# Optimization experiments

Hardware: AMD Instinct MI355X
Metric: run time of the kernel (lower is better)

The kernel has to match this reference:

```python
import jax, jax.numpy as jnp
import numpy as np

GMAX = 1.0   # args.gmax
GMIN = 0.01  # args.gmin
EPS = 0.1    # args.e_train


def setup_inputs() -> dict:
    key = jax.random.key(0)
    k1, k2, k3, k4 = jax.random.split(key, 4)
    N, B, NIN, NOUT, E = 8, 32, 128, 128, 1024
    # analog signals live in [0, 1]
    a_previous = jax.random.uniform(k1, (N, B, NIN, E), dtype=jnp.float32)
    # conductance params (clamped to [-gmax, gmax] in forward)
    theta = jax.random.uniform(k2, (NIN + 2, NOUT), dtype=jnp.float32) * 2.0 - 1.0
    # per-replica multiplicative noise seed in [0, 1); forward maps to 1 +- eps
    noise = jax.random.uniform(k3, (N, NIN + 2, NOUT), dtype=jnp.float32)
    # printed-tanh activation params eta = [offset, scale, shift, slope]
    eta = jnp.array([0.0, 1.0, 0.0, 1.0], dtype=jnp.float32) + 0.1 * jax.random.normal(k4, (4,), dtype=jnp.float32)
    return {"a_previous": a_previous, "theta": theta, "noise": noise, "eta": eta}


def reference(a_previous, theta, noise, eta):
    sg = jax.lax.stop_gradient
    # theta property: clamp + gmin pruning with straight-through estimator
    t = jnp.clip(theta, -GMAX, GMAX)
    t = jnp.where(jnp.abs(t) < GMIN, 0.0, t)
    theta_eff = sg(t) + theta - sg(theta)
    # theta_noisy: replicate over N with multiplicative uniform noise in [1-eps, 1+eps]
    theta_noisy = theta_eff[None, :, :] * ((noise * 2.0 - 1.0) * EPS + 1.0)  # [N, M, O], M = n_in+2
    # W: abs-normalized conductances per output column group
    abs_tn = jnp.abs(theta_noisy)
    W = abs_tn / (jnp.sum(abs_tn, axis=1, keepdims=True) + 1e-10)
    # sign masks (constants w.r.t. grad: values fully overwritten in torch)
    pos = sg((theta_noisy >= 0.0).astype(theta_noisy.dtype))
    neg = 1.0 - pos
    # a: [N, B, n_in, E] -> [N, B, E, n_in]; append ones and zeros columns
    a_r = jnp.transpose(a_previous, (0, 1, 3, 2))
    ones = jnp.ones(a_r.shape[:3] + (1,), a_r.dtype)
    zeros = jnp.zeros_like(ones)
    a_ext = jnp.concatenate([a_r, ones, zeros], axis=3)  # [N, B, E, M]
    # INV: unipolar complement; zero the last (zeros) column after inversion
    a_neg = (1.0 - a_ext).at[..., -1].set(0.0)
    # split-sign MAC: z [N, B, E, n_out]
    z = (jnp.einsum('nbem,nmo->nbeo', a_ext, W * pos)
         + jnp.einsum('nbem,nmo->nbeo', a_neg, W * neg))
    # printed tanh activation
    act = eta[0] + eta[1] * jnp.tanh((z - eta[2]) * eta[3])
    # back to [N, B, n_out, E]
    return jnp.transpose(act, (0, 1, 3, 2))
```

## Files before the change

kernel.cpp:

```cpp
#include <hip/hip_runtime.h>
#include <hip/hip_bf16.h>
#include <stdint.h>

#define N_REP 8
#define BATCH 32
#define NIN   128
#define NOUT  128
#define EDIM  1024
#define MDIM  130
#define ETILE 128
#define SE    130

typedef __attribute__((ext_vector_type(8))) short short8;
typedef __attribute__((ext_vector_type(4))) float f32x4;

__device__ __forceinline__ unsigned short f2bf(float f) {
    union { float f; uint32_t u; } v;
    v.f = f;
    uint32_t u = v.u;
    uint32_t r = u + 0x7fffu + ((u >> 16) & 1u);
    return (unsigned short)(r >> 16);
}

__device__ __forceinline__ uint32_t pk2bf(float lo, float hi) {
    __hip_bfloat162 h = __float22bfloat162_rn(make_float2(lo, hi));
    uint32_t d;
    __builtin_memcpy(&d, &h, 4);
    return d;
}

__global__ __launch_bounds__(64)
void prep_kernel(const float* __restrict__ theta,
                 const float* __restrict__ noise,
                 unsigned short* __restrict__ Sg,
                 float* __restrict__ biasg) {
    const int n = blockIdx.x >> 7;
    const int o = blockIdx.x & 127;
    const int lane = threadIdx.x;

    const float* nb = noise + (size_t)n * MDIM * NOUT + o;
    auto tn_at = [&](int m) -> float {
        float t = theta[m * NOUT + o];
        t = fminf(fmaxf(t, -1.f), 1.f);
        if (fabsf(t) < 0.01f) t = 0.f;
        return t * fmaf(nb[m * NOUT], 0.2f, 0.9f);
    };

    const float t0 = tn_at(lane);
    const float t1 = tn_at(lane + 64);
    const float t2 = (lane < 2) ? tn_at(128 + lane) : 0.f;

    float s = fabsf(t0) + fabsf(t1) + fabsf(t2);
#pragma unroll
    for (int d = 1; d < 64; d <<= 1) s += __shfl_xor(s, d, 64);
    const float inv = 1.f / (s + 1e-10f);

    const float w0 = fabsf(t0) * inv, w1 = fabsf(t1) * inv;
    unsigned short* srow = Sg + ((size_t)n * NOUT + o) * NIN;
    srow[lane]      = f2bf(t0 >= 0.f ? w0 : -w0);
    srow[lane + 64] = f2bf(t1 >= 0.f ? w1 : -w1);

    float b = (t0 < 0.f ? w0 : 0.f) + (t1 < 0.f ? w1 : 0.f);
    if (lane == 0 && t2 >= 0.f) b += fabsf(t2) * inv;
#pragma unroll
    for (int d = 1; d < 64; d <<= 1) b += __shfl_xor(b, d, 64);
    if (lane == 0) biasg[n * NOUT + o] = b;
}

__global__ __launch_bounds__(256, 4)
void gemm_kernel(const float* __restrict__ a,
                 const unsigned short* __restrict__ Sg,
                 const float* __restrict__ biasg,
                 const float* __restrict__ eta,
                 float* __restrict__ out) {
    __shared__ uint32_t Alds[64 * SE];
    const int bid = blockIdx.x;
    const int et  = bid & 7;
    const int nb  = bid >> 3;
    const int n   = nb >> 5;
    const int tid = threadIdx.x;

    {
        const float* abase = a + (size_t)nb * (NIN * EDIM) + et * ETILE;
        const int e4  = (tid & 31) << 2;
        const int mp0 = tid >> 5;
#pragma unroll
        for (int it = 0; it < 8; ++it) {
            const int mp = mp0 + (it << 3);
            const float4 va = *(const float4*)(abase + (size_t)(2 * mp) * EDIM + e4);
            const float4 vb = *(const float4*)(abase + (size_t)(2 * mp + 1) * EDIM + e4);
            uint2 d0, d1;
            d0.x = pk2bf(va.x, vb.x);
            d0.y = pk2bf(va.y, vb.y);
            d1.x = pk2bf(va.z, vb.z);
            d1.y = pk2bf(va.w, vb.w);
            *(uint2*)&Alds[mp * SE + e4]     = d0;
            *(uint2*)&Alds[mp * SE + e4 + 2] = d1;
        }
    }
    __syncthreads();

    const int lane = tid & 63;
    const int w = tid >> 6;
    const int r = lane & 15;
    const int q = lane >> 4;
    const int o_base = (w & 1) << 6;
    const int e_base = (w >> 1) << 6;

    f32x4 acc[4][4];
#pragma unroll
    for (int fo = 0; fo < 4; ++fo)
#pragma unroll
        for (int fe = 0; fe < 4; ++fe)
            acc[fo][fe] = (f32x4){0.f, 0.f, 0.f, 0.f};

#pragma unroll
    for (int ks = 0; ks < 4; ++ks) {
        short8 sf[4];
#pragma unroll
        for (int fo = 0; fo < 4; ++fo) {
            const int o = o_base + (fo << 4) + r;
            sf[fo] = *(const short8*)(Sg + ((size_t)(n * NOUT + o) << 7) + (ks << 5) + (q << 3));
        }
        short8 af[4];
        const int mpb = (ks << 4) + (q << 2);
#pragma unroll
        for (int fe = 0; fe < 4; ++fe) {
            const int e = e_base + (fe << 4) + r;
            uint32_t d[4];
#pragma unroll
            for (int jj = 0; jj < 4; ++jj)
                d[jj] = Alds[(mpb + jj) * SE + e];
            __builtin_memcpy(&af[fe], d, 16);
        }
#pragma unroll
        for (int fo = 0; fo < 4; ++fo)
#pragma unroll
            for (int fe = 0; fe < 4; ++fe)
                acc[fo][fe] = __builtin_amdgcn_mfma_f32_16x16x32_bf16(
                    sf[fo], af[fe], acc[fo][fe], 0, 0, 0);
    }

    const float e0 = eta[0], e1 = eta[1], e2 = eta[2], e3 = eta[3];
    float* obase = out + (size_t)nb * (NOUT * EDIM) + et * ETILE;
#pragma unroll
    for (int fo = 0; fo < 4; ++fo) {
        const int orow0 = o_base + (fo << 4) + (q << 2);
        const float4 bias4 = *(const float4*)(biasg + n * NOUT + orow0);
        const float bv[4] = {bias4.x, bias4.y, bias4.z, bias4.w};
#pragma unroll
        for (int i = 0; i < 4; ++i) {
            float* orow = obase + (size_t)(orow0 + i) * EDIM;
#pragma unroll
            for (int fe = 0; fe < 4; ++fe) {
                const float z = acc[fo][fe][i] + bv[i];
                const float y = (z - e2) * e3;
                const float ex = __expf(2.f * y);
                const float th = 1.f - 2.f * __builtin_amdgcn_rcpf(ex + 1.f);
                orow[e_base + (fe << 4) + r] = fmaf(e1, th, e0);
            }
        }
    }
}

extern "C" void kernel_launch(void* const* d_in, const int* in_sizes, int n_in,
                              void* d_out, int out_size, void* d_ws, size_t ws_size,
                              hipStream_t stream) {
    const float* a     = (const float*)d_in[0];
    const float* theta = (const float*)d_in[1];
    const float* noise = (const float*)d_in[2];
    const float* eta   = (const float*)d_in[3];
    float* out = (float*)d_out;

    unsigned short* Sg = (unsigned short*)d_ws;
    float* biasg = (float*)((char*)d_ws + (size_t)N_REP * NOUT * NIN * sizeof(unsigned short));

    prep_kernel<<<N_REP * NOUT, 64, 0, stream>>>(theta, noise, Sg, biasg);
    gemm_kernel<<<N_REP * BATCH * (EDIM / ETILE), 256, 0, stream>>>(a, Sg, biasg, eta, out);
}
```

Before: 254.3 us.

## Load A tile directly to LDS, halve E tile, vectorize output stores

Loads the fp32 activation tile with global_load_lds straight into shared memory, skipping the register round-trip, and converts to bf16 only when building MFMA fragments. ETILE is halved to 64, doubling the block count, and the MFMA operands are swapped so each lane holds four consecutive E outputs and can store them as one float4. The next k-step's weight fragments are prefetched, and bias and eta loads are hoisted ahead of the barrier. The trade-off is fp32 data in LDS (more LDS traffic, conversion inside the inner loop) and more weight reloads per output across the smaller tiles.

```diff
diff --git a/kernel.cpp b/kernel.cpp
--- a/kernel.cpp
+++ b/kernel.cpp
@@ -8,8 +8,9 @@
 #define NOUT  128
 #define EDIM  1024
 #define MDIM  130
-#define ETILE 128
-#define SE    130
+#define ETILE 64
+#define NGRP  32
+#define GSTR  260
 
 typedef __attribute__((ext_vector_type(8))) short short8;
 typedef __attribute__((ext_vector_type(4))) float f32x4;
@@ -27,6 +28,12 @@
     uint32_t d;
     __builtin_memcpy(&d, &h, 4);
     return d;
+}
+
+__device__ __forceinline__ void gload_lds16(float* lds, const float* g) {
+    __builtin_amdgcn_global_load_lds(
+        (const __attribute__((address_space(1))) void*)g,
+        (__attribute__((address_space(3))) void*)lds, 16, 0, 0);
 }
 
 __global__ __launch_bounds__(64)
@@ -73,92 +80,103 @@
                  const float* __restrict__ biasg,
                  const float* __restrict__ eta,
                  float* __restrict__ out) {
-    __shared__ uint32_t Alds[64 * SE];
-    const int bid = blockIdx.x;
-    const int et  = bid & 7;
-    const int nb  = bid >> 3;
-    const int n   = nb >> 5;
-    const int tid = threadIdx.x;
+    __shared__ float Alds[NGRP * GSTR];
+    const int bid  = blockIdx.x;
+    const int et   = bid & 15;
+    const int nb   = bid >> 4;
+    const int n    = nb >> 5;
+    const int tid  = threadIdx.x;
+    const int lane = tid & 63;
+    const int w    = tid >> 6;
+    const int r    = lane & 15;
+    const int q    = lane >> 4;
 
     {
-        const float* abase = a + (size_t)nb * (NIN * EDIM) + et * ETILE;
-        const int e4  = (tid & 31) << 2;
-        const int mp0 = tid >> 5;
+        const float* gp = a + (size_t)nb * (NIN * EDIM)
+                            + (size_t)(w * 32 + q) * EDIM + et * ETILE + (r << 2);
+        float* lp = &Alds[(w * 8) * GSTR];
 #pragma unroll
-        for (int it = 0; it < 8; ++it) {
-            const int mp = mp0 + (it << 3);
-            const float4 va = *(const float4*)(abase + (size_t)(2 * mp) * EDIM + e4);
-            const float4 vb = *(const float4*)(abase + (size_t)(2 * mp + 1) * EDIM + e4);
-            uint2 d0, d1;
-            d0.x = pk2bf(va.x, vb.x);
-            d0.y = pk2bf(va.y, vb.y);
-            d1.x = pk2bf(va.z, vb.z);
-            d1.y = pk2bf(va.w, vb.w);
-            *(uint2*)&Alds[mp * SE + e4]     = d0;
-            *(uint2*)&Alds[mp * SE + e4 + 2] = d1;
-        }
+        for (int t = 0; t < 8; ++t)
+            gload_lds16(lp + t * GSTR, gp + (size_t)(t * 4) * EDIM);
     }
-    __syncthreads();
 
-    const int lane = tid & 63;
-    const int w = tid >> 6;
-    const int r = lane & 15;
-    const int q = lane >> 4;
     const int o_base = (w & 1) << 6;
-    const int e_base = (w >> 1) << 6;
+    const int e_base = (w >> 1) << 5;
 
-    f32x4 acc[4][4];
+    const float e0 = eta[0], e1 = eta[1], e2 = eta[2], e3 = eta[3];
+    float bl[4];
+#pragma unroll
+    for (int fo = 0; fo < 4; ++fo)
+        bl[fo] = biasg[n * NOUT + o_base + (fo << 4) + r];
+
+    const unsigned short* sbase = Sg + ((size_t)(n * NOUT) << 7) + (q << 3);
+    short8 sf[4];
+#pragma unroll
+    for (int fo = 0; fo < 4; ++fo)
+        sf[fo] = *(const short8*)(sbase + ((size_t)(o_base + (fo << 4) + r) << 7));
+
+    f32x4 acc[4][2];
 #pragma unroll
     for (int fo = 0; fo < 4; ++fo)
 #pragma unroll
-        for (int fe = 0; fe < 4; ++fe)
+        for (int fe = 0; fe < 2; ++fe)
             acc[fo][fe] = (f32x4){0.f, 0.f, 0.f, 0.f};
+
+    __syncthreads();
 
 #pragma unroll
     for (int ks = 0; ks < 4; ++ks) {
-        short8 sf[4];
+        short8 sfn[4];
+        if (ks < 3) {
 #pragma unroll
-        for (int fo = 0; fo < 4; ++fo) {
-            const int o = o_base + (fo << 4) + r;
-            sf[fo] = *(const short8*)(Sg + ((size_t)(n * NOUT + o) << 7) + (ks << 5) + (q << 3));
+            for (int fo = 0; fo < 4; ++fo)
+                sfn[fo] = *(const short8*)(sbase + ((size_t)(o_base + (fo << 4) + r) << 7)
+                                                 + ((ks + 1) << 5));
         }
-        short8 af[4];
-        const int mpb = (ks << 4) + (q << 2);
+        short8 af[2];
 #pragma unroll
-        for (int fe = 0; fe < 4; ++fe) {
-            const int e = e_base + (fe << 4) + r;
+        for (int fe = 0; fe < 2; ++fe) {
+            const float* base = &Alds[(ks * 8 + q * 2) * GSTR + e_base + (fe << 4) + r];
             uint32_t d[4];
 #pragma unroll
-            for (int jj = 0; jj < 4; ++jj)
-                d[jj] = Alds[(mpb + jj) * SE + e];
+            for (int t = 0; t < 4; ++t) {
+                const int j0 = 2 * t, j1 = 2 * t + 1;
+                const float f0 = base[(j0 >> 2) * GSTR + (j0 & 3) * 64];
+                const float f1 = base[(j1 >> 2) * GSTR + (j1 & 3) * 64];
+                d[t] = pk2bf(f0, f1);
+            }
             __builtin_memcpy(&af[fe], d, 16);
         }
 #pragma unroll
         for (int fo = 0; fo < 4; ++fo)
 #pragma unroll
-            for (int fe = 0; fe < 4; ++fe)
+            for (int fe = 0; fe < 2; ++fe)
                 acc[fo][fe] = __builtin_amdgcn_mfma_f32_16x16x32_bf16(
-                    sf[fo], af[fe], acc[fo][fe], 0, 0, 0);
+                    af[fe], sf[fo], acc[fo][fe], 0, 0, 0);
+        if (ks < 3) {
+#pragma unroll
+            for (int fo = 0; fo < 4; ++fo)
+                sf[fo] = sfn[fo];
+        }
     }
 
-    const float e0 = eta[0], e1 = eta[1], e2 = eta[2], e3 = eta[3];
     float* obase = out + (size_t)nb * (NOUT * EDIM) + et * ETILE;
 #pragma unroll
     for (int fo = 0; fo < 4; ++fo) {
-        const int orow0 = o_base + (fo << 4) + (q << 2);
-        const float4 bias4 = *(const float4*)(biasg + n * NOUT + orow0);
-        const float bv[4] = {bias4.x, bias4.y, bias4.z, bias4.w};
+        float* orow = obase + (size_t)(o_base + (fo << 4) + r) * EDIM;
+        const float bv = bl[fo];
 #pragma unroll
-        for (int i = 0; i < 4; ++i) {
-            float* orow = obase + (size_t)(orow0 + i) * EDIM;
+        for (int fe = 0; fe < 2; ++fe) {
+            f32x4 res;
 #pragma unroll
-            for (int fe = 0; fe < 4; ++fe) {
-                const float z = acc[fo][fe][i] + bv[i];
+            for (int i = 0; i < 4; ++i) {
+                const float z = acc[fo][fe][i] + bv;
                 const float y = (z - e2) * e3;
                 const float ex = __expf(2.f * y);
                 const float th = 1.f - 2.f * __builtin_amdgcn_rcpf(ex + 1.f);
-                orow[e_base + (fe << 4) + r] = fmaf(e1, th, e0);
+                res[i] = fmaf(e1, th, e0);
             }
+            *(f32x4*)(orow + e_base + (fe << 4) + (q << 2)) = res;
         }
     }
 }
```

Result: slower. 261.0 us (+2.6%).
